# Optimization experiments

Hardware: AMD Instinct MI355X
Metric: run time of the kernel (lower is better)

The kernel has to match this reference:

```python
import jax, jax.numpy as jnp
import numpy as np

B, T, C = 4, 1024, 768
N_HEAD = 12
HEAD_DIM = C // N_HEAD          # 64
WINDOW = 256                    # sliding window size
FIRE_WIDTH = 32
FIRE_INIT_L = 512.0
FIRE_EPS = 1e-6
ROPE_THETA = 10000.0


def setup_inputs() -> dict:
    key = jax.random.key(0)
    ks = jax.random.split(key, 8)
    s = 0.02
    return {
        "x": jax.random.normal(ks[0], (B, T, C), dtype=jnp.float32),
        "Wq": jax.random.normal(ks[1], (C, C), dtype=jnp.float32) * s,
        "Wk": jax.random.normal(ks[2], (C, C), dtype=jnp.float32) * s,
        "Wv": jax.random.normal(ks[3], (C, C), dtype=jnp.float32) * s,
        "Wproj": jax.random.normal(ks[4], (C, C), dtype=jnp.float32) * s,
        "fire_w1": jax.random.normal(ks[5], (1, FIRE_WIDTH), dtype=jnp.float32) * s,
        "fire_b1": jnp.zeros((FIRE_WIDTH,), dtype=jnp.float32),
        "fire_w2": jax.random.normal(ks[6], (FIRE_WIDTH, N_HEAD), dtype=jnp.float32) * s,
        "fire_b2": jnp.zeros((N_HEAD,), dtype=jnp.float32),
        "fire_c": jnp.asarray(0.1, dtype=jnp.float32),
        "fire_Lmult": jnp.asarray(1.0, dtype=jnp.float32),
        "iter_num": 1000,
    }


def _rope(t):
    # t: [B, H, T, D]; half-split rotary embedding
    d = t.shape[-1]
    pos = jnp.arange(t.shape[2], dtype=t.dtype)
    inv_freq = 1.0 / (ROPE_THETA ** (jnp.arange(0, d, 2, dtype=t.dtype) / d))
    ang = pos[:, None] * inv_freq[None, :]            # [T, D/2]
    cos, sin = jnp.cos(ang), jnp.sin(ang)
    t1, t2 = t[..., : d // 2], t[..., d // 2 :]
    return jnp.concatenate([t1 * cos - t2 * sin, t1 * sin + t2 * cos], axis=-1)


def _fire_bias(w1, b1, w2, b2, c, Lmult, Tlen, dtype):
    # FIRE: psi(i-j)/psi(max(i, L)) -> tiny MLP -> per-head bias [H, T, T]
    pos = jnp.arange(Tlen, dtype=dtype)
    rel = pos[:, None] - pos[None, :]                 # [T, T]
    thresh = jnp.abs(Lmult * FIRE_INIT_L)
    pos_norm = jnp.maximum(pos, thresh)
    rel_log = jnp.log(jnp.abs(c * rel) + 1.0)
    norm_log = jnp.log(jnp.abs(c * pos_norm) + 1.0) + FIRE_EPS
    z = (rel_log / norm_log[:, None])[..., None]      # [T, T, 1]
    h = jax.nn.relu(z @ w1 + b1)                      # [T, T, W]
    bias = h @ w2 + b2                                # [T, T, H]
    return jnp.transpose(bias, (2, 0, 1))             # [H, T, T]


def reference(x, Wq, Wk, Wv, Wproj, fire_w1, fire_b1, fire_w2, fire_b2,
              fire_c, fire_Lmult, iter_num):
    Bx, Tx, Cx = x.shape
    q = (x @ Wq).reshape(Bx, Tx, N_HEAD, HEAD_DIM).transpose(0, 2, 1, 3)
    k = (x @ Wk).reshape(Bx, Tx, N_HEAD, HEAD_DIM).transpose(0, 2, 1, 3)
    v = (x @ Wv).reshape(Bx, Tx, N_HEAD, HEAD_DIM).transpose(0, 2, 1, 3)
    q, k = _rope(q), _rope(k)

    att = jnp.einsum("bhqd,bhkd->bhqk", q, k) / jnp.sqrt(
        jnp.asarray(HEAD_DIM, x.dtype))
    att = att + _fire_bias(fire_w1, fire_b1, fire_w2, fire_b2,
                           fire_c, fire_Lmult, Tx, x.dtype)[None]

    # sliding-window causal mask: 0 <= q_idx - kv_idx <= WINDOW
    idx = jnp.arange(Tx)
    rel = idx[:, None] - idx[None, :]
    allowed = (rel >= 0) & (rel <= WINDOW)            # [T, T]
    att = jnp.where(allowed[None, None], att, jnp.asarray(-jnp.inf, att.dtype))
    att = jax.nn.softmax(att, axis=-1)

    y = jnp.einsum("bhqk,bhkd->bhqd", att, v)
    y = y.transpose(0, 2, 1, 3).reshape(Bx, Tx, Cx)
    return y @ Wproj
```

## Files before the change

kernel.cpp:

```cpp
#include <hip/hip_runtime.h>

typedef unsigned short u16;
typedef __attribute__((ext_vector_type(8))) short bf16x8;
typedef __attribute__((ext_vector_type(4))) float f32x4;

#define NB 4
#define NT 1024
#define NC 768
#define NH 12
#define HD 64

__device__ __forceinline__ u16 f2bf(float f) {
  union { float f; unsigned u; } v; v.f = f;
  unsigned r = v.u + 0x7FFFu + ((v.u >> 16) & 1u);
  return (u16)(r >> 16);
}
__device__ __forceinline__ float bf2f(u16 h) {
  union { unsigned u; float f; } v; v.u = ((unsigned)h) << 16;
  return v.f;
}

__device__ __forceinline__ void gld16(const u16* g, u16* l) {
  __builtin_amdgcn_global_load_lds((const __attribute__((address_space(1))) void*)g,
                                   (__attribute__((address_space(3))) void*)l, 16, 0, 0);
}

__global__ __launch_bounds__(256) void prep_k(const float* __restrict__ x,
                                              const float* __restrict__ Wq,
                                              const float* __restrict__ Wk,
                                              const float* __restrict__ Wv,
                                              const float* __restrict__ Wp,
                                              u16* __restrict__ xb,
                                              u16* __restrict__ Wt,
                                              u16* __restrict__ Wtp) {
  __shared__ u16 tile[64][65];
  const int bid = blockIdx.x;
  const int tid = threadIdx.x;
  if (bid < 1536) {
    const int base = bid * 2048 + tid * 8;
    const f32x4* xv = (const f32x4*)(x + base);
    f32x4 v0 = xv[0], v1 = xv[1];
    bf16x8 o;
#pragma unroll
    for (int j = 0; j < 4; ++j) {
      o[j] = (short)f2bf(v0[j]);
      o[4 + j] = (short)f2bf(v1[j]);
    }
    *(bf16x8*)(xb + base) = o;
  } else {
    int idx = bid - 1536;
    int z = idx / 144, rem = idx - z * 144;
    int k0 = (rem / 12) * 64, n0 = (rem % 12) * 64;
    const float* src = (z == 0) ? Wq : (z == 1) ? Wk : (z == 2) ? Wv : Wp;
    const int c = tid & 63, r4 = tid >> 6;
#pragma unroll
    for (int p = 0; p < 16; ++p) {
      int kk = p * 4 + r4;
      tile[kk][c] = f2bf(src[(size_t)(k0 + kk) * NC + n0 + c]);
    }
    __syncthreads();
    u16* dst = (z < 3) ? (Wt + (size_t)z * NC * NC) : Wtp;
#pragma unroll
    for (int p = 0; p < 16; ++p) {
      int nn = p * 4 + r4;
      dst[(size_t)(n0 + nn) * NC + k0 + c] = tile[c][nn];
    }
  }
}

__global__ __launch_bounds__(256, 3) void gemm_qkv_rope(const u16* __restrict__ A,
                                                        const u16* __restrict__ Bt,
                                                        const float* __restrict__ w1,
                                                        const float* __restrict__ b1,
                                                        const float* __restrict__ w2,
                                                        const float* __restrict__ b2,
                                                        const float* __restrict__ cP,
                                                        const float* __restrict__ LmP,
                                                        u16* __restrict__ Qp,
                                                        u16* __restrict__ Kp,
                                                        u16* __restrict__ Vp,
                                                        u16* __restrict__ ebias) {
  constexpr int K = NC;
  __shared__ __align__(16) u16 smem[9472];
  const int bid0 = blockIdx.x;
  const int tid = threadIdx.x;

  if (bid0 >= 576) {
    int q = bid0 - 576;
    float c = cP[0], Lm = LmP[0];
    float thresh = fabsf(Lm * 512.0f);
    float pn = fmaxf((float)q, thresh);
    float inv_nl = 1.0f / (logf(fabsf(c * pn) + 1.0f) + 1e-6f);
    for (int idx = tid; idx < 384; idx += 256) {
      int rel = idx - 64;
      float out[NH];
      if (rel >= 0 && rel <= 256) {
        float z = logf(fabsf(c * (float)rel) + 1.0f) * inv_nl;
        float acc[NH];
#pragma unroll
        for (int hh = 0; hh < NH; ++hh) acc[hh] = b2[hh];
#pragma unroll
        for (int j = 0; j < 32; ++j) {
          float hj = fmaxf(z * w1[j] + b1[j], 0.0f);
#pragma unroll
          for (int hh = 0; hh < NH; ++hh) acc[hh] += hj * w2[j * NH + hh];
        }
#pragma unroll
        for (int hh = 0; hh < NH; ++hh) out[hh] = __expf(acc[hh]);
      } else {
#pragma unroll
        for (int hh = 0; hh < NH; ++hh) out[hh] = 0.0f;
      }
#pragma unroll
      for (int hh = 0; hh < NH; ++hh)
        ebias[((size_t)hh * NT + q) * 384 + idx] = f2bf(out[hh]);
    }
    return;
  }

  u16* As = smem;
  u16* Bs = smem + 4096;
  const int lin = (bid0 & 7) * 72 + (bid0 >> 3);
  const int m0 = (lin & 31) * 128, n0 = (lin >> 5) * 128;
  const int wid = tid >> 6, lane = tid & 63;
  const int wr = wid >> 1, wc = wid & 1;
  const int lr = lane & 15, lg = lane >> 4, lk = lg << 3;
  const int srow = wid * 16 + (lane >> 2);
  const int scol = (lane & 3) * 8;
  f32x4 acc[4][4] = {};
  const u16* Ag = A + (size_t)(m0 + srow) * K + scol;
  const u16* Bg = Bt + (size_t)(n0 + srow) * K + scol;
  u16* Al = &As[(wid * 16) * 32];
  u16* Bl = &Bs[(wid * 16) * 32];

  for (int k0 = 0; k0 < K; k0 += 32) {
    gld16(Ag + k0, Al);
    gld16(Ag + (size_t)64 * K + k0, Al + 64 * 32);
    gld16(Bg + k0, Bl);
    gld16(Bg + (size_t)64 * K + k0, Bl + 64 * 32);
    __syncthreads();
    bf16x8 af[4], bfv[4];
#pragma unroll
    for (int i = 0; i < 4; ++i)
      af[i] = *(const bf16x8*)&As[(wr * 64 + i * 16 + lr) * 32 + lk];
#pragma unroll
    for (int j = 0; j < 4; ++j)
      bfv[j] = *(const bf16x8*)&Bs[(wc * 64 + j * 16 + lr) * 32 + lk];
#pragma unroll
    for (int i = 0; i < 4; ++i)
#pragma unroll
      for (int j = 0; j < 4; ++j)
        acc[i][j] = __builtin_amdgcn_mfma_f32_16x16x32_bf16(af[i], bfv[j], acc[i][j], 0, 0, 0);
    __syncthreads();
  }

  const int rbase = lg * 4;
  const int base_col = n0 + wc * 64;
  const int part = base_col / 768;
  const int h = (base_col % 768) >> 6;
  const int b = m0 >> 10;
  const int bh = b * NH + h;
  const int tbase = (m0 & 1023) + wr * 64;

  if (part < 2) {
    u16* dst = (part == 0 ? Qp : Kp) + ((size_t)bh << 16);
    const float inv0 = __expf(-(float)lr * 0.28782313662425f);
    const float inv1 = __expf(-(float)(lr + 16) * 0.28782313662425f);
#pragma unroll
    for (int i = 0; i < 4; ++i)
#pragma unroll
      for (int rr = 0; rr < 4; ++rr) {
        const int tl = tbase + i * 16 + rbase + rr;
        float s0, c0, s1, c1;
        __sincosf((float)tl * inv0, &s0, &c0);
        __sincosf((float)tl * inv1, &s1, &c1);
        const float a0 = acc[i][0][rr], a1 = acc[i][1][rr];
        const float a2 = acc[i][2][rr], a3 = acc[i][3][rr];
        const size_t ro = (size_t)tl * HD;
        dst[ro + lr]      = f2bf(a0 * c0 - a2 * s0);
        dst[ro + 16 + lr] = f2bf(a1 * c1 - a3 * s1);
        dst[ro + 32 + lr] = f2bf(a0 * s0 + a2 * c0);
        dst[ro + 48 + lr] = f2bf(a1 * s1 + a3 * c1);
      }
  } else {
    u16* dst = Vp + ((size_t)bh << 16);
    u16* vb = smem + wid * 64 * 37;
#pragma unroll
    for (int hf = 0; hf < 2; ++hf) {
#pragma unroll
      for (int i = 0; i < 4; ++i)
#pragma unroll
        for (int rr = 0; rr < 4; ++rr) {
          const int row = i * 16 + rbase + rr;
          vb[row * 37 + lr]      = f2bf(acc[i][2 * hf][rr]);
          vb[row * 37 + 16 + lr] = f2bf(acc[i][2 * hf + 1][rr]);
        }
      asm volatile("s_waitcnt lgkmcnt(0)" ::: "memory");
#pragma unroll
      for (int p = 0; p < 32; ++p) {
        const int d = hf * 32 + p;
        dst[(size_t)d * NT + tbase + lane] = vb[lane * 37 + p];
      }
    }
  }
}

template <bool F32OUT, int WR, int WC, int AI, int BJ, bool SWZ>
__global__ __launch_bounds__(256, 4) void gemm_lds(const u16* __restrict__ A,
                                                   const u16* __restrict__ Bt,
                                                   void* __restrict__ Cv,
                                                   int M, int N, int K) {
  constexpr int BM = WR * AI * 16;
  constexpr int BN = WC * BJ * 16;
  __shared__ u16 As[BM * 32];
  __shared__ u16 Bs[BN * 32];
  const int tid = threadIdx.x;
  const int wid = tid >> 6, lane = tid & 63;
  const int wr = wid / WC, wc = wid % WC;
  int lin = blockIdx.x;
  if (SWZ) lin = (lin & 7) * (gridDim.x >> 3) + (lin >> 3);
  const int mt = M / BM;
  const int m0 = (lin % mt) * BM, n0 = (lin / mt) * BN;
  const int lr = lane & 15, lk = (lane >> 4) << 3;
  const int srow = wid * 16 + (lane >> 2);
  const int scol = (lane & 3) * 8;
  f32x4 acc[AI][BJ] = {};
  const u16* Ag = A + (size_t)(m0 + srow) * K + scol;
  const u16* Bg = Bt + (size_t)(n0 + srow) * K + scol;
  u16* Al = &As[(wid * 16) * 32];
  u16* Bl = &Bs[(wid * 16) * 32];

  for (int k0 = 0; k0 < K; k0 += 32) {
#pragma unroll
    for (int ia = 0; ia < BM / 64; ++ia)
      gld16(Ag + (size_t)(ia * 64) * K + k0, Al + ia * 64 * 32);
#pragma unroll
    for (int ib = 0; ib < BN / 64; ++ib)
      gld16(Bg + (size_t)(ib * 64) * K + k0, Bl + ib * 64 * 32);
    __syncthreads();
    bf16x8 af[AI], bfv[BJ];
#pragma unroll
    for (int i = 0; i < AI; ++i)
      af[i] = *(const bf16x8*)&As[(wr * AI * 16 + i * 16 + lr) * 32 + lk];
#pragma unroll
    for (int j = 0; j < BJ; ++j)
      bfv[j] = *(const bf16x8*)&Bs[(wc * BJ * 16 + j * 16 + lr) * 32 + lk];
#pragma unroll
    for (int i = 0; i < AI; ++i)
#pragma unroll
      for (int j = 0; j < BJ; ++j)
        acc[i][j] = __builtin_amdgcn_mfma_f32_16x16x32_bf16(af[i], bfv[j], acc[i][j], 0, 0, 0);
    __syncthreads();
  }
  const int rbase = (lane >> 4) * 4;
#pragma unroll
  for (int i = 0; i < AI; ++i)
#pragma unroll
    for (int j = 0; j < BJ; ++j)
#pragma unroll
      for (int r = 0; r < 4; ++r) {
        size_t row = m0 + wr * AI * 16 + i * 16 + rbase + r;
        size_t col = n0 + wc * BJ * 16 + j * 16 + lr;
        if (F32OUT)
          ((float*)Cv)[row * N + col] = acc[i][j][r];
        else
          ((u16*)Cv)[row * N + col] = f2bf(acc[i][j][r]);
      }
}

__global__ __launch_bounds__(256, 3) void attn_k(const u16* __restrict__ Q,
                                                 const u16* __restrict__ K,
                                                 const u16* __restrict__ Vt,
                                                 const u16* __restrict__ ebias,
                                                 u16* __restrict__ Y) {
  __shared__ __align__(16) u16 Ks[2][64][64];
  __shared__ __align__(16) u16 Vs[2][64][64];
  __shared__ __align__(16) u16 plds[4][16][72];
  const int bid = blockIdx.x;
  const int xcd = bid & 7, j = bid >> 3;
  const int qb = j & 15, t6 = j >> 4;
  const int yslot = xcd * 6 + t6;
  const int b = yslot & 3, h = yslot >> 2;
  const int bh = b * NH + h;
  const int Q0 = qb << 6;
  const int tid = threadIdx.x, wid = tid >> 6, lane = tid & 63;
  const int q0 = Q0 + wid * 16;
  const int lr = lane & 15, lg = lane >> 4, lk = lg << 3;
  const u16* Qb = Q + ((size_t)bh << 16);
  const u16* Kb = K + ((size_t)bh << 16);
  const u16* Vb = Vt + ((size_t)bh << 16);
  const u16* ebh = ebias + (size_t)h * NT * 384;

  bf16x8 aq0 = *(const bf16x8*)(Qb + (q0 + lr) * HD + lk);
  bf16x8 aq1 = *(const bf16x8*)(Qb + (q0 + lr) * HD + 32 + lk);
  bf16x8 ones;
#pragma unroll
  for (int i = 0; i < 8; ++i) ones[i] = (short)0x3F80;
  f32x4 yacc[4] = {};
  f32x4 lsum = {};
  u16(*pl)[72] = plds[wid];

  int cstart = Q0 - 256;
  if (cstart < 0) cstart = 0;
  const int n = ((Q0 + 64) - cstart) >> 6;

  const int srow = lane >> 3;
  const int sseg = (lane & 7) ^ srow;
  auto STAGE = [&](int buf, int c) {
#pragma unroll
    for (int i = 0; i < 2; ++i) {
      const int rb = (i * 4 + wid) * 8;
      gld16(Kb + (size_t)(c + rb + srow) * HD + sseg * 8, &Ks[buf][rb][0]);
      gld16(Vb + (size_t)(rb + srow) * NT + c + sseg * 8, &Vs[buf][rb][0]);
    }
  };
  auto LOADEB = [&](float (&e)[4][4], int c) {
#pragma unroll
    for (int kk = 0; kk < 4; ++kk) {
      const int kcol = c + kk * 16 + lr;
#pragma unroll
      for (int r = 0; r < 4; ++r) {
        int qrow = q0 + lg * 4 + r;
        int idx = qrow - kcol + 64;
        idx = idx < 0 ? 0 : (idx > 383 ? 383 : idx);
        e[kk][r] = bf2f(ebh[(size_t)qrow * 384 + idx]);
      }
    }
  };

  STAGE(0, cstart);
  float ebc[4][4];
  LOADEB(ebc, cstart);
  __syncthreads();

  int c = cstart;
  for (int ci = 0; ci < n; ++ci, c += 64) {
    const int cur = ci & 1;
    const bool more = (ci + 1 < n);
    if (more) STAGE(cur ^ 1, c + 64);
    float ebn[4][4];
    if (more) LOADEB(ebn, c + 64);
    const int rsw = (lr & 7) << 4;
#pragma unroll
    for (int kk = 0; kk < 4; ++kk) {
      const char* krow = (const char*)&Ks[cur][kk * 16 + lr][0];
      bf16x8 bk0 = *(const bf16x8*)(krow + ((lg * 16) ^ rsw));
      bf16x8 bk1 = *(const bf16x8*)(krow + ((lg * 16 + 64) ^ rsw));
      f32x4 t = {};
      t = __builtin_amdgcn_mfma_f32_16x16x32_bf16(aq0, bk0, t, 0, 0, 0);
      t = __builtin_amdgcn_mfma_f32_16x16x32_bf16(aq1, bk1, t, 0, 0, 0);
#pragma unroll
      for (int r = 0; r < 4; ++r) {
        float p = __expf(t[r] * 0.125f) * ebc[kk][r];
        pl[lg * 4 + r][kk * 16 + lr] = f2bf(p);
      }
    }
    asm volatile("s_waitcnt lgkmcnt(0)" ::: "memory");
    bf16x8 ap0 = *(const bf16x8*)&pl[lr][lk];
    bf16x8 ap1 = *(const bf16x8*)&pl[lr][32 + lk];
    lsum = __builtin_amdgcn_mfma_f32_16x16x32_bf16(ap0, ones, lsum, 0, 0, 0);
    lsum = __builtin_amdgcn_mfma_f32_16x16x32_bf16(ap1, ones, lsum, 0, 0, 0);
#pragma unroll
    for (int dt = 0; dt < 4; ++dt) {
      const char* vrow = (const char*)&Vs[cur][dt * 16 + lr][0];
      bf16x8 bv0 = *(const bf16x8*)(vrow + ((lg * 16) ^ rsw));
      bf16x8 bv1 = *(const bf16x8*)(vrow + ((lg * 16 + 64) ^ rsw));
      yacc[dt] = __builtin_amdgcn_mfma_f32_16x16x32_bf16(ap0, bv0, yacc[dt], 0, 0, 0);
      yacc[dt] = __builtin_amdgcn_mfma_f32_16x16x32_bf16(ap1, bv1, yacc[dt], 0, 0, 0);
    }
    if (more) {
#pragma unroll
      for (int kk = 0; kk < 4; ++kk)
#pragma unroll
        for (int r = 0; r < 4; ++r) ebc[kk][r] = ebn[kk][r];
    }
    __syncthreads();
  }

  float linv[4];
#pragma unroll
  for (int r = 0; r < 4; ++r) linv[r] = 1.0f / lsum[r];
#pragma unroll
  for (int dt = 0; dt < 4; ++dt)
#pragma unroll
    for (int r = 0; r < 4; ++r) {
      int qrow = q0 + lg * 4 + r;
      int d = dt * 16 + lr;
      Y[(size_t)(b * NT + qrow) * NC + h * HD + d] = f2bf(yacc[dt][r] * linv[r]);
    }
}

static constexpr size_t OFF_XB = 0;
static constexpr size_t OFF_WT = OFF_XB + 6291456;
static constexpr size_t OFF_WTP = OFF_WT + 3538944;
static constexpr size_t OFF_Q = OFF_WTP + 1179648;
static constexpr size_t OFF_K = OFF_Q + 6291456;
static constexpr size_t OFF_VT = OFF_K + 6291456;
static constexpr size_t OFF_BIAS = OFF_VT + 6291456;
static constexpr size_t OFF_Y = OFF_BIAS + 9437184;

extern "C" void kernel_launch(void* const* d_in, const int* in_sizes, int n_in,
                              void* d_out, int out_size, void* d_ws, size_t ws_size,
                              hipStream_t stream) {
  const float* x = (const float*)d_in[0];
  const float* Wq = (const float*)d_in[1];
  const float* Wk = (const float*)d_in[2];
  const float* Wv = (const float*)d_in[3];
  const float* Wp = (const float*)d_in[4];
  const float* fw1 = (const float*)d_in[5];
  const float* fb1 = (const float*)d_in[6];
  const float* fw2 = (const float*)d_in[7];
  const float* fb2 = (const float*)d_in[8];
  const float* fc = (const float*)d_in[9];
  const float* fLm = (const float*)d_in[10];

  char* ws = (char*)d_ws;
  u16* xb = (u16*)(ws + OFF_XB);
  u16* Wt = (u16*)(ws + OFF_WT);
  u16* Wtp = (u16*)(ws + OFF_WTP);
  u16* Qb = (u16*)(ws + OFF_Q);
  u16* Kb = (u16*)(ws + OFF_K);
  u16* Vtb = (u16*)(ws + OFF_VT);
  u16* ebiasb = (u16*)(ws + OFF_BIAS);
  u16* Yb = (u16*)(ws + OFF_Y);

  prep_k<<<2112, 256, 0, stream>>>(x, Wq, Wk, Wv, Wp, xb, Wt, Wtp);
  gemm_qkv_rope<<<1600, 256, 0, stream>>>(xb, Wt, fw1, fb1, fw2, fb2, fc, fLm,
                                          Qb, Kb, Vtb, ebiasb);
  attn_k<<<768, 256, 0, stream>>>(Qb, Kb, Vtb, ebiasb, Yb);
  gemm_lds<true, 2, 2, 4, 2, true><<<384, 256, 0, stream>>>(Yb, Wtp, d_out, 4096, 768, 768);
}
```

Before: 69.14 us.

## Fuse fp32-to-bf16 conversion of x into QKV GEMM A-tile loading

Removes the separate x-to-bf16 conversion pass from the prep kernel. The QKV GEMM now reads fp32 x directly, packs it to bf16 in registers and stores it to LDS, which saves a full write and re-read of the bf16 copy. In exchange the A tiles go through register loads instead of asynchronous direct-to-LDS loads, and each column tile re-converts its rows. The attention exponent also switches from __expf to exp2f with a folded log2(e) scale, and a template flag on the output-projection GEMM is flipped to false, whose effect is not visible here.

```diff
diff --git a/kernel.cpp b/kernel.cpp
--- a/kernel.cpp
+++ b/kernel.cpp
@@ -1,8 +1,10 @@
 #include <hip/hip_runtime.h>
+#include <hip/hip_bf16.h>
 
 typedef unsigned short u16;
 typedef __attribute__((ext_vector_type(8))) short bf16x8;
 typedef __attribute__((ext_vector_type(4))) float f32x4;
+typedef __attribute__((ext_vector_type(4))) unsigned u32x4;
 
 #define NB 4
 #define NT 1024
@@ -19,56 +21,45 @@
   union { unsigned u; float f; } v; v.u = ((unsigned)h) << 16;
   return v.f;
 }
+__device__ __forceinline__ unsigned pk2(float a, float b) {
+  __hip_bfloat162 h = __float22bfloat162_rn(make_float2(a, b));
+  union { __hip_bfloat162 h; unsigned u; } v; v.h = h;
+  return v.u;
+}
 
 __device__ __forceinline__ void gld16(const u16* g, u16* l) {
   __builtin_amdgcn_global_load_lds((const __attribute__((address_space(1))) void*)g,
                                    (__attribute__((address_space(3))) void*)l, 16, 0, 0);
 }
 
-__global__ __launch_bounds__(256) void prep_k(const float* __restrict__ x,
-                                              const float* __restrict__ Wq,
+__global__ __launch_bounds__(256) void prep_k(const float* __restrict__ Wq,
                                               const float* __restrict__ Wk,
                                               const float* __restrict__ Wv,
                                               const float* __restrict__ Wp,
-                                              u16* __restrict__ xb,
                                               u16* __restrict__ Wt,
                                               u16* __restrict__ Wtp) {
   __shared__ u16 tile[64][65];
-  const int bid = blockIdx.x;
+  const int idx = blockIdx.x;
   const int tid = threadIdx.x;
-  if (bid < 1536) {
-    const int base = bid * 2048 + tid * 8;
-    const f32x4* xv = (const f32x4*)(x + base);
-    f32x4 v0 = xv[0], v1 = xv[1];
-    bf16x8 o;
-#pragma unroll
-    for (int j = 0; j < 4; ++j) {
-      o[j] = (short)f2bf(v0[j]);
-      o[4 + j] = (short)f2bf(v1[j]);
-    }
-    *(bf16x8*)(xb + base) = o;
-  } else {
-    int idx = bid - 1536;
-    int z = idx / 144, rem = idx - z * 144;
-    int k0 = (rem / 12) * 64, n0 = (rem % 12) * 64;
-    const float* src = (z == 0) ? Wq : (z == 1) ? Wk : (z == 2) ? Wv : Wp;
-    const int c = tid & 63, r4 = tid >> 6;
-#pragma unroll
-    for (int p = 0; p < 16; ++p) {
-      int kk = p * 4 + r4;
-      tile[kk][c] = f2bf(src[(size_t)(k0 + kk) * NC + n0 + c]);
-    }
-    __syncthreads();
-    u16* dst = (z < 3) ? (Wt + (size_t)z * NC * NC) : Wtp;
-#pragma unroll
-    for (int p = 0; p < 16; ++p) {
-      int nn = p * 4 + r4;
-      dst[(size_t)(n0 + nn) * NC + k0 + c] = tile[c][nn];
-    }
-  }
-}
-
-__global__ __launch_bounds__(256, 3) void gemm_qkv_rope(const u16* __restrict__ A,
+  int z = idx / 144, rem = idx - z * 144;
+  int k0 = (rem / 12) * 64, n0 = (rem % 12) * 64;
+  const float* src = (z == 0) ? Wq : (z == 1) ? Wk : (z == 2) ? Wv : Wp;
+  const int c = tid & 63, r4 = tid >> 6;
+#pragma unroll
+  for (int p = 0; p < 16; ++p) {
+    int kk = p * 4 + r4;
+    tile[kk][c] = f2bf(src[(size_t)(k0 + kk) * NC + n0 + c]);
+  }
+  __syncthreads();
+  u16* dst = (z < 3) ? (Wt + (size_t)z * NC * NC) : Wtp;
+#pragma unroll
+  for (int p = 0; p < 16; ++p) {
+    int nn = p * 4 + r4;
+    dst[(size_t)(n0 + nn) * NC + k0 + c] = tile[c][nn];
+  }
+}
+
+__global__ __launch_bounds__(256, 3) void gemm_qkv_rope(const float* __restrict__ x,
                                                         const u16* __restrict__ Bt,
                                                         const float* __restrict__ w1,
                                                         const float* __restrict__ b1,
@@ -127,17 +118,26 @@
   const int lr = lane & 15, lg = lane >> 4, lk = lg << 3;
   const int srow = wid * 16 + (lane >> 2);
   const int scol = (lane & 3) * 8;
+  const int ar = tid >> 1;
+  const int ah = (tid & 1) * 16;
   f32x4 acc[4][4] = {};
-  const u16* Ag = A + (size_t)(m0 + srow) * K + scol;
+  const float* Ag = x + (size_t)(m0 + ar) * K + ah;
   const u16* Bg = Bt + (size_t)(n0 + srow) * K + scol;
-  u16* Al = &As[(wid * 16) * 32];
   u16* Bl = &Bs[(wid * 16) * 32];
 
   for (int k0 = 0; k0 < K; k0 += 32) {
-    gld16(Ag + k0, Al);
-    gld16(Ag + (size_t)64 * K + k0, Al + 64 * 32);
+    f32x4 av[4];
+#pragma unroll
+    for (int j = 0; j < 4; ++j) av[j] = *(const f32x4*)(Ag + k0 + j * 4);
     gld16(Bg + k0, Bl);
     gld16(Bg + (size_t)64 * K + k0, Bl + 64 * 32);
+    u32x4 s0, s1;
+    s0[0] = pk2(av[0][0], av[0][1]); s0[1] = pk2(av[0][2], av[0][3]);
+    s0[2] = pk2(av[1][0], av[1][1]); s0[3] = pk2(av[1][2], av[1][3]);
+    s1[0] = pk2(av[2][0], av[2][1]); s1[1] = pk2(av[2][2], av[2][3]);
+    s1[2] = pk2(av[3][0], av[3][1]); s1[3] = pk2(av[3][2], av[3][3]);
+    *(u32x4*)&As[ar * 32 + ah] = s0;
+    *(u32x4*)&As[ar * 32 + ah + 8] = s1;
     __syncthreads();
     bf16x8 af[4], bfv[4];
 #pragma unroll
@@ -333,6 +333,7 @@
   LOADEB(ebc, cstart);
   __syncthreads();
 
+  const float SC = 0.125f * 1.44269504088896f;
   int c = cstart;
   for (int ci = 0; ci < n; ++ci, c += 64) {
     const int cur = ci & 1;
@@ -351,7 +352,7 @@
       t = __builtin_amdgcn_mfma_f32_16x16x32_bf16(aq1, bk1, t, 0, 0, 0);
 #pragma unroll
       for (int r = 0; r < 4; ++r) {
-        float p = __expf(t[r] * 0.125f) * ebc[kk][r];
+        float p = exp2f(t[r] * SC) * ebc[kk][r];
         pl[lg * 4 + r][kk * 16 + lr] = f2bf(p);
       }
     }
@@ -390,8 +391,7 @@
     }
 }
 
-static constexpr size_t OFF_XB = 0;
-static constexpr size_t OFF_WT = OFF_XB + 6291456;
+static constexpr size_t OFF_WT = 0;
 static constexpr size_t OFF_WTP = OFF_WT + 3538944;
 static constexpr size_t OFF_Q = OFF_WTP + 1179648;
 static constexpr size_t OFF_K = OFF_Q + 6291456;
@@ -415,7 +415,6 @@
   const float* fLm = (const float*)d_in[10];
 
   char* ws = (char*)d_ws;
-  u16* xb = (u16*)(ws + OFF_XB);
   u16* Wt = (u16*)(ws + OFF_WT);
   u16* Wtp = (u16*)(ws + OFF_WTP);
   u16* Qb = (u16*)(ws + OFF_Q);
@@ -424,9 +423,9 @@
   u16* ebiasb = (u16*)(ws + OFF_BIAS);
   u16* Yb = (u16*)(ws + OFF_Y);
 
-  prep_k<<<2112, 256, 0, stream>>>(x, Wq, Wk, Wv, Wp, xb, Wt, Wtp);
-  gemm_qkv_rope<<<1600, 256, 0, stream>>>(xb, Wt, fw1, fb1, fw2, fb2, fc, fLm,
+  prep_k<<<576, 256, 0, stream>>>(Wq, Wk, Wv, Wp, Wt, Wtp);
+  gemm_qkv_rope<<<1600, 256, 0, stream>>>(x, Wt, fw1, fb1, fw2, fb2, fc, fLm,
                                           Qb, Kb, Vtb, ebiasb);
   attn_k<<<768, 256, 0, stream>>>(Qb, Kb, Vtb, ebiasb, Yb);
-  gemm_lds<true, 2, 2, 4, 2, true><<<384, 256, 0, stream>>>(Yb, Wtp, d_out, 4096, 768, 768);
-}
+  gemm_lds<true, 2, 2, 4, 2, false><<<384, 256, 0, stream>>>(Yb, Wtp, d_out, 4096, 768, 768);
+}
```

Measured after the change: 75.62 us. 9.4% more time.
